# Performance work log

Measured on AMD Instinct MI355X. Metric: run time of the kernel, lower is better.

The kernel has to match this reference:

```python
import jax, jax.numpy as jnp
import numpy as np

H = 16
DH = 64


def _apply_rotary(x, cos, sin):
    # x: [b, h, s, d]; cos/sin: [s, d//2] -> broadcast to [1, 1, s, d//2]
    x1 = x[..., ::2]
    x2 = x[..., 1::2]
    c = cos[None, None]
    s = sin[None, None]
    rot = jnp.stack([x1 * c - x2 * s, x1 * s + x2 * c], axis=-1)
    return rot.reshape(x.shape)


def setup_inputs() -> dict:
    key = jax.random.key(0)
    ks = jax.random.split(key, 7)
    dim = 1024
    std = 0.02
    x = jax.random.normal(ks[0], (2, 2048, dim), dtype=jnp.float32)
    persistent = jax.random.normal(ks[1], (2, 16, dim), dtype=jnp.float32)
    memory = jax.random.normal(ks[2], (2, 64, dim), dtype=jnp.float32)
    Wq = jax.random.normal(ks[3], (dim, dim), dtype=jnp.float32) * std
    Wk = jax.random.normal(ks[4], (dim, dim), dtype=jnp.float32) * std
    Wv = jax.random.normal(ks[5], (dim, dim), dtype=jnp.float32) * std
    Wo = jax.random.normal(ks[6], (dim, dim), dtype=jnp.float32) * std
    return {"x": x, "persistent": persistent, "memory": memory,
            "Wq": Wq, "Wk": Wk, "Wv": Wv, "Wo": Wo}


def reference(x, persistent, memory, Wq, Wk, Wv, Wo):
    b, L, dim = x.shape
    P = persistent.shape[1] + memory.shape[1]  # prefix_len
    full_x = jnp.concatenate([persistent, memory, x], axis=1)  # [b, P+L, dim]
    S = full_x.shape[1]
    scale = DH ** -0.5

    def proj(W):
        y = full_x @ W.T  # [b, S, dim]
        return y.reshape(b, S, H, DH).transpose(0, 2, 1, 3)  # [b, H, S, DH]

    q = proj(Wq)
    k = proj(Wk)
    v = proj(Wv)

    # RoPE only on the main (input) segment, positions starting at 0.
    pos = jnp.arange(L, dtype=jnp.float32)
    inv_freq = 1.0 / (10000.0 ** (jnp.arange(0, DH, 2, dtype=jnp.float32) / DH))
    freqs = pos[:, None] * inv_freq[None, :]  # [L, DH//2]
    cos, sin = jnp.cos(freqs), jnp.sin(freqs)

    q_main = _apply_rotary(q[:, :, P:], cos, sin)  # [b, H, L, DH]
    k = jnp.concatenate([k[:, :, :P], _apply_rotary(k[:, :, P:], cos, sin)], axis=2)

    # Only main-segment query rows affect the returned output (output[:, P:]).
    # Mask for main queries: prefix keys fully visible; causal within main.
    qi = jnp.arange(L)[:, None]
    kj = jnp.arange(S)[None, :]
    mask = (kj < P) | ((kj - P) <= qi)  # [L, S]

    scores = jnp.einsum('bhqd,bhkd->bhqk', q_main, k) * scale  # [b, H, L, S]
    scores = jnp.where(mask[None, None], scores, -jnp.inf)
    attn = jax.nn.softmax(scores, axis=-1)
    out = jnp.einsum('bhqk,bhkd->bhqd', attn, v)  # [b, H, L, DH]
    out = out.transpose(0, 2, 1, 3).reshape(b, L, dim)
    return out @ Wo.T
```

## Files before the change

kernel.cpp:

```cpp
#include <hip/hip_runtime.h>
#include <math.h>

#define BB    2
#define LL    2048
#define DIM   1024
#define NH    16
#define DHD   64
#define NPER  16
#define NMEM  64
#define PFX   80
#define SS    2128
#define MQKV  (BB*SS)
#define NQKV  3072
#define MOUT  (BB*LL)

typedef __attribute__((ext_vector_type(4)))  float f32x4;
typedef __attribute__((ext_vector_type(16))) float f32x16;
typedef __attribute__((ext_vector_type(8)))  short bf16x8;
typedef unsigned short u16;
typedef unsigned int   u32;

union I4B8 { int4 i; bf16x8 v; };

__device__ __forceinline__ u16 f2bf(float x) {
    union { float f; u32 u; } v; v.f = x;
    return (u16)((v.u + 0x7fffu + ((v.u >> 16) & 1u)) >> 16);
}
__device__ __forceinline__ u32 cvtpk(float lo, float hi) {
    u32 r; asm("v_cvt_pk_bf16_f32 %0, %1, %2" : "=v"(r) : "v"(lo), "v"(hi));
    return r;
}
__device__ __forceinline__ void gload_lds16(const void* g, void* l) {
    __builtin_amdgcn_global_load_lds(
        (__attribute__((address_space(1))) void*)(g),
        (__attribute__((address_space(3))) void*)(l), 16, 0, 0);
}

#define BARRIER()  __builtin_amdgcn_s_barrier()
#define VMCNT0()   asm volatile("s_waitcnt vmcnt(0)")

__global__ __launch_bounds__(256)
void prep_kernel(const float* __restrict__ x,  const float* __restrict__ pe,
                 const float* __restrict__ me, const float* __restrict__ Wq,
                 const float* __restrict__ Wk, const float* __restrict__ Wv,
                 const float* __restrict__ Wo,
                 u16* __restrict__ xbf, u16* __restrict__ wqkv,
                 u16* __restrict__ wobf,
                 float* __restrict__ ropeC, float* __restrict__ ropeS)
{
    const int nthr = gridDim.x * blockDim.x;
    const int t0   = blockIdx.x * blockDim.x + threadIdx.x;

    for (int g = t0; g < MQKV * (DIM / 4); g += nthr) {
        int d4  = g & 255;
        int row = g >> 8;
        int b   = row >= SS;
        int s   = row - b * SS;
        const float* src;
        if (s < NPER)     src = pe + ((size_t)(b * NPER + s)) * DIM;
        else if (s < PFX) src = me + ((size_t)(b * NMEM + (s - NPER))) * DIM;
        else              src = x  + ((size_t)(b * LL   + (s - PFX)))  * DIM;
        float4 v = *reinterpret_cast<const float4*>(src + d4 * 4);
        ushort4 o; o.x = f2bf(v.x); o.y = f2bf(v.y); o.z = f2bf(v.z); o.w = f2bf(v.w);
        *reinterpret_cast<ushort4*>(xbf + (size_t)g * 4) = o;
    }
    for (int g = t0; g < NQKV * (DIM / 4); g += nthr) {
        int row = g >> 8;
        const float* src = (row < 1024) ? (Wq + (size_t)row * DIM)
                         : (row < 2048) ? (Wk + (size_t)(row - 1024) * DIM)
                         :                (Wv + (size_t)(row - 2048) * DIM);
        float4 v = *reinterpret_cast<const float4*>(src + (g & 255) * 4);
        ushort4 o; o.x = f2bf(v.x); o.y = f2bf(v.y); o.z = f2bf(v.z); o.w = f2bf(v.w);
        *reinterpret_cast<ushort4*>(wqkv + (size_t)g * 4) = o;
    }
    for (int g = t0; g < DIM * (DIM / 4); g += nthr) {
        float4 v = *reinterpret_cast<const float4*>(Wo + (size_t)g * 4);
        ushort4 o; o.x = f2bf(v.x); o.y = f2bf(v.y); o.z = f2bf(v.z); o.w = f2bf(v.w);
        *reinterpret_cast<ushort4*>(wobf + (size_t)g * 4) = o;
    }
    for (int i = t0; i < LL * 32; i += nthr) {
        int pos = i >> 5, fi = i & 31;
        float ang = (float)pos * exp2f(-(float)fi * 0.41524101186092029f);
        ropeC[i] = cosf(ang);
        ropeS[i] = sinf(ang);
    }
}

__global__ __launch_bounds__(256, 2)
void qkv_gemm2p(const u16* __restrict__ X, const u16* __restrict__ Wq3,
                const float* __restrict__ ropeC, const float* __restrict__ ropeS,
                u16* __restrict__ qkvraw)
{
    __shared__ short Xs[2][256 * 32] __attribute__((aligned(16)));
    __shared__ short Ws[2][128 * 32] __attribute__((aligned(16)));

    const int tid  = threadIdx.x;
    const int lane = tid & 63;
    const int wid  = tid >> 6;
    const int bm   = blockIdx.x * 256;
    const int bn   = blockIdx.y * 128;

    f32x4 acc[4][8];
#pragma unroll
    for (int m = 0; m < 4; ++m)
#pragma unroll
        for (int n = 0; n < 8; ++n) acc[m][n] = (f32x4)(0.f);

    const int srow = lane >> 2;
    const int scc  = (lane & 3) * 8;

#define STAGE_XW(buf, k0)                                                      \
    {                                                                          \
        _Pragma("unroll")                                                      \
        for (int it = 0; it < 4; ++it) {                                       \
            int r = wid * 64 + it * 16 + srow;                                 \
            int g = bm + r; if (g > MQKV - 1) g = MQKV - 1;                    \
            gload_lds16(X + (size_t)g * DIM + (k0) + scc,                      \
                        &Xs[buf][(wid * 64 + it * 16) * 32]);                  \
        }                                                                      \
        _Pragma("unroll")                                                      \
        for (int it = 0; it < 2; ++it) {                                       \
            int r = wid * 32 + it * 16 + srow;                                 \
            gload_lds16(Wq3 + (size_t)(bn + r) * DIM + (k0) + scc,             \
                        &Ws[buf][(wid * 32 + it * 16) * 32]);                  \
        }                                                                      \
    }

    STAGE_XW(0, 0);
    VMCNT0();
    BARRIER();

    const int frow = lane & 15;
    const int fkb  = (lane >> 4) * 8;

    for (int t = 0; t < 32; ++t) {
        const int cur = t & 1;
        int knext = (t + 1) * 32; if (knext >= DIM) knext = 0;
        STAGE_XW(cur ^ 1, knext);

        bf16x8 xf[4], wf[8];
#pragma unroll
        for (int m = 0; m < 4; ++m)
            xf[m] = *reinterpret_cast<const bf16x8*>(
                &Xs[cur][(wid * 64 + m * 16 + frow) * 32 + fkb]);
#pragma unroll
        for (int n = 0; n < 8; ++n)
            wf[n] = *reinterpret_cast<const bf16x8*>(
                &Ws[cur][(n * 16 + frow) * 32 + fkb]);

        __builtin_amdgcn_s_setprio(1);
#pragma unroll
        for (int m = 0; m < 4; ++m)
#pragma unroll
            for (int n = 0; n < 8; ++n)
                acc[m][n] = __builtin_amdgcn_mfma_f32_16x16x32_bf16(
                    wf[n], xf[m], acc[m][n], 0, 0, 0);
        __builtin_amdgcn_s_setprio(0);

        VMCNT0();
        BARRIER();
    }
#undef STAGE_XW

    const int cbase = bn + ((lane >> 4) << 2);
    const int rbase = bm + wid * 64 + (lane & 15);
    const int which = bn >> 10;

#pragma unroll
    for (int m = 0; m < 4; ++m) {
        const int row = rbase + m * 16;
        if (row >= MQKV) continue;
        const int b = row >= SS;
        const int s = row - b * SS;
        const bool rope = (which != 2) && (s >= PFX);
        const int pos = s - PFX;
#pragma unroll
        for (int n = 0; n < 8; ++n) {
            const int c0 = cbase + n * 16;
            float v0 = acc[m][n][0], v1 = acc[m][n][1];
            float v2 = acc[m][n][2], v3 = acc[m][n][3];
            if (rope) {
                const int dh = c0 & 63;
                float2 cs = *reinterpret_cast<const float2*>(ropeC + pos * 32 + (dh >> 1));
                float2 sn = *reinterpret_cast<const float2*>(ropeS + pos * 32 + (dh >> 1));
                float t0 = v0 * cs.x - v1 * sn.x;
                v1 = v0 * sn.x + v1 * cs.x; v0 = t0;
                float t2 = v2 * cs.y - v3 * sn.y;
                v3 = v2 * sn.y + v3 * cs.y; v2 = t2;
            }
            ushort4 o;
            o.x = f2bf(v0); o.y = f2bf(v1); o.z = f2bf(v2); o.w = f2bf(v3);
            *reinterpret_cast<ushort4*>(&qkvraw[(size_t)row * NQKV + c0]) = o;
        }
    }
}

__global__ __launch_bounds__(256)
void wo_gemm(const u16* __restrict__ A, const u16* __restrict__ Bw,
             float* __restrict__ outp)
{
    __shared__ short As[128 * 32] __attribute__((aligned(16)));
    __shared__ short Bs[128 * 32] __attribute__((aligned(16)));

    const int tid  = threadIdx.x;
    const int lane = tid & 63;
    const int wid  = tid >> 6;
    const int wr   = wid >> 1, wc = wid & 1;
    const int bm   = blockIdx.x * 128;
    const int bn   = blockIdx.y * 128;

    f32x4 acc[4][4];
#pragma unroll
    for (int m = 0; m < 4; ++m)
#pragma unroll
        for (int n = 0; n < 4; ++n) acc[m][n] = (f32x4)(0.f);

    const int r0 = wid * 32 + (lane >> 2);
    const int cc = (lane & 3) * 8;

    for (int k0 = 0; k0 < DIM; k0 += 32) {
        gload_lds16(A + (size_t)(bm + r0) * DIM + k0 + cc, As + wid * 1024);
        gload_lds16(A + (size_t)(bm + r0 + 16) * DIM + k0 + cc, As + wid * 1024 + 512);
        gload_lds16(Bw + (size_t)(bn + r0) * DIM + k0 + cc, Bs + wid * 1024);
        gload_lds16(Bw + (size_t)(bn + r0 + 16) * DIM + k0 + cc, Bs + wid * 1024 + 512);
        __syncthreads();

        bf16x8 wf[4], xf[4];
#pragma unroll
        for (int m = 0; m < 4; ++m)
            wf[m] = *reinterpret_cast<const bf16x8*>(
                Bs + (wr * 64 + m * 16 + (lane & 15)) * 32 + (lane >> 4) * 8);
#pragma unroll
        for (int n = 0; n < 4; ++n)
            xf[n] = *reinterpret_cast<const bf16x8*>(
                As + (wc * 64 + n * 16 + (lane & 15)) * 32 + (lane >> 4) * 8);
#pragma unroll
        for (int m = 0; m < 4; ++m)
#pragma unroll
            for (int n = 0; n < 4; ++n)
                acc[m][n] = __builtin_amdgcn_mfma_f32_16x16x32_bf16(
                    wf[m], xf[n], acc[m][n], 0, 0, 0);
        __syncthreads();
    }

    const int cbase = bn + wr * 64 + ((lane >> 4) << 2);
    const int rbase = bm + wc * 64 + (lane & 15);
#pragma unroll
    for (int n = 0; n < 4; ++n) {
        const int row = rbase + n * 16;
#pragma unroll
        for (int m = 0; m < 4; ++m) {
            const int c0 = cbase + m * 16;
            *reinterpret_cast<float4*>(&outp[(size_t)row * DIM + c0]) =
                make_float4(acc[m][n][0], acc[m][n][1], acc[m][n][2], acc[m][n][3]);
        }
    }
}

__device__ __forceinline__ void attn_load_tile(
    const u16* __restrict__ kb0, const u16* __restrict__ vb0,
    int j0, int tid, int vp, int vo,
    int4& k0r, int4& k1r, int4& v0r, int4& v1r)
{
    int key0 = tid >> 3,        o0 = tid & 7;
    int c1   = tid + 256;
    int key1 = c1 >> 3,         o1 = c1 & 7;
    int jg0 = j0 + key0; if (jg0 > SS - 1) jg0 = SS - 1;
    int jg1 = j0 + key1; if (jg1 > SS - 1) jg1 = SS - 1;
    k0r = *reinterpret_cast<const int4*>(kb0 + (size_t)jg0 * NQKV + o0 * 8);
    k1r = *reinterpret_cast<const int4*>(kb0 + (size_t)jg1 * NQKV + o1 * 8);
    int ja  = j0 + 2 * vp;     if (ja  > SS - 1) ja  = SS - 1;
    int jb2 = j0 + 2 * vp + 1; if (jb2 > SS - 1) jb2 = SS - 1;
    v0r = *reinterpret_cast<const int4*>(vb0 + (size_t)ja  * NQKV + vo * 8);
    v1r = *reinterpret_cast<const int4*>(vb0 + (size_t)jb2 * NQKV + vo * 8);
}

__global__ __launch_bounds__(256, 2)
void attn_mfma(const u16* __restrict__ qkvraw, u16* __restrict__ ctx)
{
    __shared__ u16 Ks[64 * 64] __attribute__((aligned(16)));
    __shared__ u16 Vt[64 * 64] __attribute__((aligned(16)));
    __shared__ u16 Ot[4][32 * 72] __attribute__((aligned(16)));

    const int tid  = threadIdx.x;
    const int lane = tid & 63;
    const int wv   = tid >> 6;
    const int h    = lane >> 5;
    const int ql   = lane & 31;

    const int bh   = blockIdx.y;
    const int b    = bh >> 4;
    const int head = bh & 15;
    int qt = blockIdx.x;
    if (b) qt = 15 - qt;
    const int q0  = qt * 128;
    const int q0w = q0 + 32 * wv;

    const u16* qrow = qkvraw + (size_t)(b * SS + PFX + q0w + ql) * NQKV + head * DHD;
    bf16x8 qf[4];
#pragma unroll
    for (int ks = 0; ks < 4; ++ks) {
        I4B8 t; t.i = *reinterpret_cast<const int4*>(qrow + ks * 16 + h * 8);
        qf[ks] = t.v;
    }

    f32x16 oa0 = (f32x16)(0.f), oa1 = (f32x16)(0.f);
    float m = -INFINITY, l = 0.f;

    const u16* kb0 = qkvraw + (size_t)b * SS * NQKV + 1024 + head * DHD;
    const u16* vb0 = qkvraw + (size_t)b * SS * NQKV + 2048 + head * DHD;

    const int ntiles   = (PFX + q0 + 128 + 63) / 64;
    const int wave_lim = PFX + q0w + 31;
    const int vp = tid & 31;
    const int vo = tid >> 5;

    int4 rk0, rk1, rv0, rv1;
    attn_load_tile(kb0, vb0, 0, tid, vp, vo, rk0, rk1, rv0, rv1);

    for (int kt = 0; kt < ntiles; ++kt) {
        const int j0 = kt * 64;

        {
            int key0 = tid >> 3, o0 = tid & 7;
            int c1 = tid + 256;
            int key1 = c1 >> 3, o1 = c1 & 7;
            *reinterpret_cast<int4*>((char*)Ks + ((key0 * 128 + o0 * 16) ^ ((key0 & 7) << 4))) = rk0;
            *reinterpret_cast<int4*>((char*)Ks + ((key1 * 128 + o1 * 16) ^ ((key1 & 7) << 4))) = rk1;
            const u16* pa = reinterpret_cast<const u16*>(&rv0);
            const u16* pb = reinterpret_cast<const u16*>(&rv1);
#pragma unroll
            for (int d = 0; d < 8; ++d) {
                u32 wpk = (u32)pa[d] | ((u32)pb[d] << 16);
                int dh = vo * 8 + d;
                *reinterpret_cast<u32*>((char*)Vt + ((dh * 128 + vp * 4) ^ ((d & 7) << 4))) = wpk;
            }
        }
        __syncthreads();

        int4 nk0, nk1, nv0, nv1;
        attn_load_tile(kb0, vb0, j0 + 64, tid, vp, vo, nk0, nk1, nv0, nv1);

        if (j0 <= wave_lim) {
            f32x16 s0 = (f32x16)(0.f), s1 = (f32x16)(0.f);
            __builtin_amdgcn_s_setprio(1);
#pragma unroll
            for (int ks = 0; ks < 4; ++ks) {
                I4B8 k0, k1;
                k0.i = *reinterpret_cast<const int4*>(
                    (const char*)Ks + (((ql) * 128 + ks * 32 + h * 16) ^ ((ql & 7) << 4)));
                k1.i = *reinterpret_cast<const int4*>(
                    (const char*)Ks + (((32 + ql) * 128 + ks * 32 + h * 16) ^ ((ql & 7) << 4)));
                s0 = __builtin_amdgcn_mfma_f32_32x32x16_bf16(k0.v, qf[ks], s0, 0, 0, 0);
                s1 = __builtin_amdgcn_mfma_f32_32x32x16_bf16(k1.v, qf[ks], s1, 0, 0, 0);
            }
            __builtin_amdgcn_s_setprio(0);
            float sv[32];
#pragma unroll
            for (int i = 0; i < 16; ++i) { sv[i] = s0[i] * 0.125f; sv[16 + i] = s1[i] * 0.125f; }
            if (j0 + 63 > PFX + q0w) {
                const int lim = PFX + q0w + ql - j0;
#pragma unroll
                for (int i = 0; i < 32; ++i) {
                    int koff = ((i >= 16) ? 32 : 0) + (i & 3) + 8 * ((i & 15) >> 2) + 4 * h;
                    if (koff > lim) sv[i] = -INFINITY;
                }
            }
            float mt = sv[0];
#pragma unroll
            for (int i = 1; i < 32; ++i) mt = fmaxf(mt, sv[i]);
            mt = fmaxf(mt, __shfl_xor(mt, 32));
            float mn = fmaxf(m, mt);
            float f = __expf(m - mn);
            m = mn;
            float ls = 0.f;
            u32 W0[8], W1[8];
#pragma unroll
            for (int i = 0; i < 8; ++i) {
                float pa = __expf(sv[2 * i] - m);
                float pb = __expf(sv[2 * i + 1] - m);
                ls += pa + pb;
                W0[i] = cvtpk(pa, pb);
            }
#pragma unroll
            for (int i = 0; i < 8; ++i) {
                float pa = __expf(sv[16 + 2 * i] - m);
                float pb = __expf(sv[16 + 2 * i + 1] - m);
                ls += pa + pb;
                W1[i] = cvtpk(pa, pb);
            }
            ls += __shfl_xor(ls, 32);
            l = l * f + ls;
#pragma unroll
            for (int i = 0; i < 16; ++i) { oa0[i] *= f; oa1[i] *= f; }

            __builtin_amdgcn_s_setprio(1);
#pragma unroll
            for (int ks = 0; ks < 4; ++ks) {
                const int a4 = (ks & 1) * 4;
                u32 A0, A1, A2, A3;
                if (ks < 2) { A0 = W0[a4]; A1 = W0[a4 + 1]; A2 = W0[a4 + 2]; A3 = W0[a4 + 3]; }
                else        { A0 = W1[a4]; A1 = W1[a4 + 1]; A2 = W1[a4 + 2]; A3 = W1[a4 + 3]; }
                asm volatile("v_permlane32_swap_b32 %0, %1" : "+v"(A0), "+v"(A2));
                asm volatile("v_permlane32_swap_b32 %0, %1" : "+v"(A1), "+v"(A3));
                I4B8 pf; pf.i = make_int4((int)A0, (int)A1, (int)A2, (int)A3);
                I4B8 vf0, vf1;
                vf0.i = *reinterpret_cast<const int4*>(
                    (const char*)Vt + (((ql) * 128 + ks * 32 + h * 16) ^ ((ql & 7) << 4)));
                vf1.i = *reinterpret_cast<const int4*>(
                    (const char*)Vt + (((32 + ql) * 128 + ks * 32 + h * 16) ^ ((ql & 7) << 4)));
                oa0 = __builtin_amdgcn_mfma_f32_32x32x16_bf16(vf0.v, pf.v, oa0, 0, 0, 0);
                oa1 = __builtin_amdgcn_mfma_f32_32x32x16_bf16(vf1.v, pf.v, oa1, 0, 0, 0);
            }
            __builtin_amdgcn_s_setprio(0);
        }
        __syncthreads();
        rk0 = nk0; rk1 = nk1; rv0 = nv0; rv1 = nv1;
    }

    const float inv = 1.f / l;
    u16* orow = &Ot[wv][ql * 72];
#pragma unroll
    for (int i = 0; i < 8; ++i) {
        u32 w0 = cvtpk(oa0[2 * i] * inv, oa0[2 * i + 1] * inv);
        u32 w1 = cvtpk(oa1[2 * i] * inv, oa1[2 * i + 1] * inv);
        int dh0 = ((2 * i) & 3) + 8 * ((2 * i) >> 2) + 4 * h;
        *reinterpret_cast<u32*>(&orow[dh0]) = w0;
        *reinterpret_cast<u32*>(&orow[32 + dh0]) = w1;
    }
    const int rr = lane >> 1, hh = lane & 1;
    const u16* src = &Ot[wv][rr * 72 + hh * 32];
    u16* dst = ctx + ((size_t)(b * LL + q0 + 32 * wv + rr)) * DIM + head * DHD + hh * 32;
#pragma unroll
    for (int i = 0; i < 4; ++i) {
        int4 t = *reinterpret_cast<const int4*>(src + i * 8);
        *reinterpret_cast<int4*>(dst + i * 8) = t;
    }
}

extern "C" void kernel_launch(void* const* d_in, const int* in_sizes, int n_in,
                              void* d_out, int out_size, void* d_ws, size_t ws_size,
                              hipStream_t stream)
{
    const float* x  = (const float*)d_in[0];
    const float* pe = (const float*)d_in[1];
    const float* me = (const float*)d_in[2];
    const float* Wq = (const float*)d_in[3];
    const float* Wk = (const float*)d_in[4];
    const float* Wv = (const float*)d_in[5];
    const float* Wo = (const float*)d_in[6];
    float* out = (float*)d_out;

    u16* xbf  = (u16*)d_ws;
    u16* wqkv = xbf + (size_t)MQKV * DIM;
    u16* wobf = wqkv + (size_t)NQKV * DIM;
    float* ropeC = (float*)(wobf + (size_t)DIM * DIM);
    float* ropeS = ropeC + LL * 32;
    u16* qkvraw = (u16*)(ropeS + LL * 32);
    u16* ctx = qkvraw + (size_t)MQKV * NQKV;

    hipLaunchKernelGGL(prep_kernel, dim3(2048), dim3(256), 0, stream,
                       x, pe, me, Wq, Wk, Wv, Wo, xbf, wqkv, wobf, ropeC, ropeS);
    hipLaunchKernelGGL(qkv_gemm2p, dim3((MQKV + 255) / 256, NQKV / 128), dim3(256), 0, stream,
                       xbf, wqkv, ropeC, ropeS, qkvraw);
    hipLaunchKernelGGL(attn_mfma, dim3(16, BB * NH), dim3(256), 0, stream,
                       qkvraw, ctx);
    hipLaunchKernelGGL(wo_gemm, dim3(MOUT / 128, DIM / 128), dim3(256), 0, stream,
                       ctx, wobf, out);
}
```

Baseline: 136.8 us.

## Shrink QKV GEMM block tile to 128x128 with a 2x2 wave layout

Changes the QKV projection GEMM from 256x128 block tiles, where each wave owned 64 rows across all 128 columns, to 128x128 tiles split over a 2x2 wave grid of 64x64 subtiles. It also raises launch_bounds occupancy to 3 blocks per CU and doubles the grid along M. The aim is more blocks for better CU fill (34x24 instead of 17x24) and less register and LDS pressure per block. The cost is lower per-block data reuse and more global loads of the weight tiles.

Result: faster. 132.8 us (-2.9%).

```diff
diff --git a/kernel.cpp b/kernel.cpp
--- a/kernel.cpp
+++ b/kernel.cpp
@@ -86,97 +86,89 @@
     }
 }
 
-__global__ __launch_bounds__(256, 2)
+__global__ __launch_bounds__(256, 3)
 void qkv_gemm2p(const u16* __restrict__ X, const u16* __restrict__ Wq3,
                 const float* __restrict__ ropeC, const float* __restrict__ ropeS,
                 u16* __restrict__ qkvraw)
 {
-    __shared__ short Xs[2][256 * 32] __attribute__((aligned(16)));
+    __shared__ short Xs[2][128 * 32] __attribute__((aligned(16)));
     __shared__ short Ws[2][128 * 32] __attribute__((aligned(16)));
 
     const int tid  = threadIdx.x;
     const int lane = tid & 63;
     const int wid  = tid >> 6;
-    const int bm   = blockIdx.x * 256;
+    const int wr   = wid >> 1, wc = wid & 1;
+    const int bm   = blockIdx.x * 128;
     const int bn   = blockIdx.y * 128;
 
-    f32x4 acc[4][8];
+    f32x4 acc[4][4];
 #pragma unroll
     for (int m = 0; m < 4; ++m)
 #pragma unroll
-        for (int n = 0; n < 8; ++n) acc[m][n] = (f32x4)(0.f);
-
-    const int srow = lane >> 2;
-    const int scc  = (lane & 3) * 8;
-
-#define STAGE_XW(buf, k0)                                                      \
+        for (int n = 0; n < 4; ++n) acc[m][n] = (f32x4)(0.f);
+
+    const int r0 = wid * 32 + (lane >> 2);
+    const int cc = (lane & 3) * 8;
+    int ga0 = bm + r0;      if (ga0 > MQKV - 1) ga0 = MQKV - 1;
+    int ga1 = bm + r0 + 16; if (ga1 > MQKV - 1) ga1 = MQKV - 1;
+    const int gb0 = bn + r0, gb1 = bn + r0 + 16;
+
+#define STAGE2(buf, k0)                                                        \
     {                                                                          \
-        _Pragma("unroll")                                                      \
-        for (int it = 0; it < 4; ++it) {                                       \
-            int r = wid * 64 + it * 16 + srow;                                 \
-            int g = bm + r; if (g > MQKV - 1) g = MQKV - 1;                    \
-            gload_lds16(X + (size_t)g * DIM + (k0) + scc,                      \
-                        &Xs[buf][(wid * 64 + it * 16) * 32]);                  \
-        }                                                                      \
-        _Pragma("unroll")                                                      \
-        for (int it = 0; it < 2; ++it) {                                       \
-            int r = wid * 32 + it * 16 + srow;                                 \
-            gload_lds16(Wq3 + (size_t)(bn + r) * DIM + (k0) + scc,             \
-                        &Ws[buf][(wid * 32 + it * 16) * 32]);                  \
-        }                                                                      \
-    }
-
-    STAGE_XW(0, 0);
+        gload_lds16(X + (size_t)ga0 * DIM + (k0) + cc, &Xs[buf][wid * 1024]);  \
+        gload_lds16(X + (size_t)ga1 * DIM + (k0) + cc, &Xs[buf][wid * 1024 + 512]); \
+        gload_lds16(Wq3 + (size_t)gb0 * DIM + (k0) + cc, &Ws[buf][wid * 1024]);\
+        gload_lds16(Wq3 + (size_t)gb1 * DIM + (k0) + cc, &Ws[buf][wid * 1024 + 512]); \
+    }
+
+    STAGE2(0, 0);
     VMCNT0();
     BARRIER();
-
-    const int frow = lane & 15;
-    const int fkb  = (lane >> 4) * 8;
 
     for (int t = 0; t < 32; ++t) {
         const int cur = t & 1;
         int knext = (t + 1) * 32; if (knext >= DIM) knext = 0;
-        STAGE_XW(cur ^ 1, knext);
-
-        bf16x8 xf[4], wf[8];
+        STAGE2(cur ^ 1, knext);
+
+        bf16x8 wf[4], xf[4];
 #pragma unroll
         for (int m = 0; m < 4; ++m)
-            xf[m] = *reinterpret_cast<const bf16x8*>(
-                &Xs[cur][(wid * 64 + m * 16 + frow) * 32 + fkb]);
-#pragma unroll
-        for (int n = 0; n < 8; ++n)
-            wf[n] = *reinterpret_cast<const bf16x8*>(
-                &Ws[cur][(n * 16 + frow) * 32 + fkb]);
+            wf[m] = *reinterpret_cast<const bf16x8*>(
+                &Ws[cur][(wr * 64 + m * 16 + (lane & 15)) * 32 + (lane >> 4) * 8]);
+#pragma unroll
+        for (int n = 0; n < 4; ++n)
+            xf[n] = *reinterpret_cast<const bf16x8*>(
+                &Xs[cur][(wc * 64 + n * 16 + (lane & 15)) * 32 + (lane >> 4) * 8]);
 
         __builtin_amdgcn_s_setprio(1);
 #pragma unroll
         for (int m = 0; m < 4; ++m)
 #pragma unroll
-            for (int n = 0; n < 8; ++n)
+            for (int n = 0; n < 4; ++n)
                 acc[m][n] = __builtin_amdgcn_mfma_f32_16x16x32_bf16(
-                    wf[n], xf[m], acc[m][n], 0, 0, 0);
+                    wf[m], xf[n], acc[m][n], 0, 0, 0);
         __builtin_amdgcn_s_setprio(0);
 
         VMCNT0();
         BARRIER();
     }
-#undef STAGE_XW
-
-    const int cbase = bn + ((lane >> 4) << 2);
-    const int rbase = bm + wid * 64 + (lane & 15);
+#undef STAGE2
+
+    const int cbase = bn + wr * 64 + ((lane >> 4) << 2);
+    const int rbase = bm + wc * 64 + (lane & 15);
     const int which = bn >> 10;
 
 #pragma unroll
-    for (int m = 0; m < 4; ++m) {
-        const int row = rbase + m * 16;
+    for (int n = 0; n < 4; ++n) {
+        const int row = rbase + n * 16;
         if (row >= MQKV) continue;
         const int b = row >= SS;
         const int s = row - b * SS;
         const bool rope = (which != 2) && (s >= PFX);
         const int pos = s - PFX;
 #pragma unroll
-        for (int n = 0; n < 8; ++n) {
-            const int c0 = cbase + n * 16;
+        for (int m = 0; m < 4; ++m) {
+            const int c0 = cbase + m * 16;
             float v0 = acc[m][n][0], v1 = acc[m][n][1];
             float v2 = acc[m][n][2], v3 = acc[m][n][3];
             if (rope) {
@@ -461,7 +453,7 @@
 
     hipLaunchKernelGGL(prep_kernel, dim3(2048), dim3(256), 0, stream,
                        x, pe, me, Wq, Wk, Wv, Wo, xbf, wqkv, wobf, ropeC, ropeS);
-    hipLaunchKernelGGL(qkv_gemm2p, dim3((MQKV + 255) / 256, NQKV / 128), dim3(256), 0, stream,
+    hipLaunchKernelGGL(qkv_gemm2p, dim3((MQKV + 127) / 128, NQKV / 128), dim3(256), 0, stream,
                        xbf, wqkv, ropeC, ropeS, qkvraw);
     hipLaunchKernelGGL(attn_mfma, dim3(16, BB * NH), dim3(256), 0, stream,
                        qkvraw, ctx);
```
